# Optimization experiments

Hardware: AMD Instinct MI355X
Metric: run time of the kernel (lower is better)

Reference implementation:

```python
import jax, jax.numpy as jnp
import numpy as np

B, P, E = 16, 1024, 768
HID, HEADS = 768, 12
DH = HID // HEADS  # 64
EPS = 1e-5


def setup_inputs() -> dict:
    key = jax.random.key(0)
    ks = jax.random.split(key, 4)
    return {
        "x": jax.random.normal(ks[0], (B, P, E), dtype=jnp.float32),
        "ln_weight": jnp.ones((P, E), dtype=jnp.float32),
        "ln_bias": jnp.zeros((P, E), dtype=jnp.float32),
        "qkv": jax.random.normal(ks[1], (E, 3 * HID), dtype=jnp.float32),
        "lin_w": jax.random.normal(ks[2], (HID, E), dtype=jnp.float32) * 0.02,
        "lin_b": jax.random.normal(ks[3], (E,), dtype=jnp.float32) * 0.02,
    }


def reference(x, ln_weight, ln_bias, qkv, lin_w, lin_b):
    # LayerNorm over the last TWO dims (patches, emb), per torch nn.LayerNorm((P, E))
    mean = jnp.mean(x, axis=(-2, -1), keepdims=True)
    var = jnp.var(x, axis=(-2, -1), keepdims=True)
    xn = (x - mean) / jnp.sqrt(var + EPS) * ln_weight + ln_bias

    # QKV projection: [B,P,E] @ [E,3*HID] -> [B,P,3*HID]
    proj = xn @ qkv
    # view(B,P,heads,-1) then permute -> [B,heads,P,3*DH]; chunk along last dim
    proj = proj.reshape(B, P, HEADS, 3 * DH).transpose(0, 2, 1, 3)
    q, k, v = proj[..., :DH], proj[..., DH:2 * DH], proj[..., 2 * DH:]

    # Softmax-free attention: (Q K^T) V
    atten = jnp.einsum("bhqd,bhkd->bhqk", q, k)  # [B,H,P,P]
    out = jnp.einsum("bhqk,bhkd->bhqd", atten, v)  # [B,H,P,DH]

    out = out.transpose(0, 2, 1, 3).reshape(B, P, HID)
    # dropout p=0.0 (eval) -> identity
    out = jax.nn.relu(out @ lin_w + lin_b)
    return out + x
```

## Files before the change

kernel.cpp:

```cpp
#include <hip/hip_runtime.h>
#include <hip/hip_bf16.h>
#include <cstdint>

#define BB   16
#define PP   1024
#define EE   768
#define HID  768
#define NH   12
#define DH   64
#define NPB  (PP * EE)
#define MROWS (BB * PP)

typedef __bf16 bf16_t;
typedef __bf16 bf16x8 __attribute__((ext_vector_type(8)));
typedef float  f32x4  __attribute__((ext_vector_type(4)));

__device__ __forceinline__ void gld16(const void* g, void* l) {
    __builtin_amdgcn_global_load_lds(
        (const __attribute__((address_space(1))) void*)(uintptr_t)g,
        (__attribute__((address_space(3))) void*)(uint32_t)(uintptr_t)l,
        16, 0, 0);
}

__global__ __launch_bounds__(256) void stats1_kernel(const float* __restrict__ x,
                                                     float* __restrict__ part) {
    int bid = blockIdx.x;
    int b = bid >> 6, s = bid & 63;
    const float4* xp = (const float4*)(x + (size_t)b * NPB + (size_t)s * 12288);
    float sum = 0.f, ss = 0.f;
#pragma unroll
    for (int i = 0; i < 12; ++i) {
        float4 v = xp[i * 256 + threadIdx.x];
        sum += v.x + v.y + v.z + v.w;
        ss  += v.x * v.x + v.y * v.y + v.z * v.z + v.w * v.w;
    }
#pragma unroll
    for (int off = 32; off > 0; off >>= 1) {
        sum += __shfl_down(sum, off, 64);
        ss  += __shfl_down(ss,  off, 64);
    }
    __shared__ float tmp[8];
    int wave = threadIdx.x >> 6, lane = threadIdx.x & 63;
    if (lane == 0) { tmp[wave * 2] = sum; tmp[wave * 2 + 1] = ss; }
    __syncthreads();
    if (threadIdx.x == 0) {
        part[bid * 2]     = tmp[0] + tmp[2] + tmp[4] + tmp[6];
        part[bid * 2 + 1] = tmp[1] + tmp[3] + tmp[5] + tmp[7];
    }
}

__global__ __launch_bounds__(256) void prep_kernel(const float* __restrict__ qkvw,
                                                   const float* __restrict__ linw,
                                                   bf16_t* __restrict__ qkvT,
                                                   bf16_t* __restrict__ lwT) {
    int bid = blockIdx.x;
    __shared__ float lds[64][65];
    const float* src; bf16_t* dst; int r0, c0, W;
    if (bid < 432) {
        int tr = bid / 36, tc = bid - tr * 36;
        r0 = tr * 64; c0 = tc * 64; src = qkvw; W = 2304; dst = qkvT;
    } else {
        int bb = bid - 432;
        int tr = bb / 12, tc = bb - tr * 12;
        r0 = tr * 64; c0 = tc * 64; src = linw; W = 768; dst = lwT;
    }
    int t = threadIdx.x;
    int rr = t >> 4, cc4 = (t & 15) * 4;
#pragma unroll
    for (int j = 0; j < 4; ++j) {
        float4 v = *(const float4*)(src + (size_t)(r0 + rr + j * 16) * W + c0 + cc4);
        lds[rr + j * 16][cc4 + 0] = v.x;
        lds[rr + j * 16][cc4 + 1] = v.y;
        lds[rr + j * 16][cc4 + 2] = v.z;
        lds[rr + j * 16][cc4 + 3] = v.w;
    }
    __syncthreads();
    int cl = t >> 3, rgl = (t & 7) * 8;
#pragma unroll
    for (int jj = 0; jj < 2; ++jj) {
        int c = jj * 32 + cl;
        union { bf16_t h[8]; uint4 u; } o;
#pragma unroll
        for (int k = 0; k < 8; ++k) o.h[k] = (bf16_t)lds[rgl + k][c];
        *(uint4*)(dst + (size_t)(c0 + c) * 768 + r0 + rgl) = o.u;
    }
}

__global__ __launch_bounds__(256) void ln_apply_kernel(const float* __restrict__ x,
                                                       const float* __restrict__ lnw,
                                                       const float* __restrict__ lnb,
                                                       const float* __restrict__ part,
                                                       bf16_t* __restrict__ xn) {
    int i = (blockIdx.x * 256 + threadIdx.x) * 8;
    int b = i / NPB;
    int r = i - b * NPB;
    int lane = threadIdx.x & 63;
    float sum = part[(b * 64 + lane) * 2];
    float ss  = part[(b * 64 + lane) * 2 + 1];
#pragma unroll
    for (int off = 32; off > 0; off >>= 1) {
        sum += __shfl_down(sum, off, 64);
        ss  += __shfl_down(ss,  off, 64);
    }
    const float inv_n = 1.f / (float)NPB;
    float mean = __shfl(sum, 0, 64) * inv_n;
    float var  = __shfl(ss,  0, 64) * inv_n - mean * mean;
    float rstd = rsqrtf(var + 1e-5f);

    float4 x0 = *(const float4*)(x + i),     x1 = *(const float4*)(x + i + 4);
    float4 w0 = *(const float4*)(lnw + r),   w1 = *(const float4*)(lnw + r + 4);
    float4 c0 = *(const float4*)(lnb + r),   c1 = *(const float4*)(lnb + r + 4);
    union { bf16_t h[8]; uint4 u; } o;
    o.h[0] = (bf16_t)((x0.x - mean) * rstd * w0.x + c0.x);
    o.h[1] = (bf16_t)((x0.y - mean) * rstd * w0.y + c0.y);
    o.h[2] = (bf16_t)((x0.z - mean) * rstd * w0.z + c0.z);
    o.h[3] = (bf16_t)((x0.w - mean) * rstd * w0.w + c0.w);
    o.h[4] = (bf16_t)((x1.x - mean) * rstd * w1.x + c1.x);
    o.h[5] = (bf16_t)((x1.y - mean) * rstd * w1.y + c1.y);
    o.h[6] = (bf16_t)((x1.z - mean) * rstd * w1.z + c1.z);
    o.h[7] = (bf16_t)((x1.w - mean) * rstd * w1.w + c1.w);
    *(uint4*)(xn + i) = o.u;
}

__device__ __forceinline__ void core128_bk32(const bf16_t* __restrict__ A,
                                             const bf16_t* __restrict__ Bt,
                                             int mBase, int nBase,
                                             f32x4 acc[4][4], bf16_t* smem) {
    const int t = threadIdx.x, lane = t & 63, wave = t >> 6;
    const int wm = wave >> 1, wn = wave & 1;
    const int m16 = lane & 15, quad = lane >> 4;

    const bf16_t* gsrc[4];
    int ldst[4];
#pragma unroll
    for (int j = 0; j < 2; ++j) {
        int c = t + 256 * j;
        int l = c >> 3, lg = ((c & 7) - (l & 7)) & 7;
        int row = l + (lg >> 2) * 64, kc = lg & 3;
        gsrc[j]     = A  + (size_t)(mBase + row) * 768 + kc * 8;
        ldst[j]     = c * 8;
        gsrc[2 + j] = Bt + (size_t)(nBase + row) * 768 + kc * 8;
        ldst[2 + j] = 4096 + c * 8;
    }

    int aOff[4], bOff[4];
#pragma unroll
    for (int f = 0; f < 4; ++f) {
        aOff[f] = (f * 16 + m16) * 64 + (((wm * 4 + quad) + (m16 & 7)) & 7) * 8;
        bOff[f] = 4096 + (f * 16 + m16) * 64 + (((wn * 4 + quad) + (m16 & 7)) & 7) * 8;
    }

    const f32x4 z = {0.f, 0.f, 0.f, 0.f};
#pragma unroll
    for (int mf = 0; mf < 4; ++mf)
#pragma unroll
        for (int nf = 0; nf < 4; ++nf) acc[mf][nf] = z;

#pragma unroll
    for (int j = 0; j < 4; ++j) gld16(gsrc[j], smem + ldst[j]);
#pragma unroll
    for (int j = 0; j < 4; ++j) gld16(gsrc[j] + 32, smem + 8192 + ldst[j]);

#pragma unroll
    for (int step = 0; step < 24; ++step) {
        const int cur = (step % 3) * 8192;
        asm volatile("s_waitcnt lgkmcnt(0)" ::: "memory");
        __builtin_amdgcn_sched_barrier(0);
        __builtin_amdgcn_s_barrier();
        if (step + 2 < 24) {
            const int nb = ((step + 2) % 3) * 8192;
            const int kq = (step + 2) * 32;
#pragma unroll
            for (int j = 0; j < 4; ++j)
                gld16(gsrc[j] + kq, smem + nb + ldst[j]);
        }
        if (step < 22)       asm volatile("s_waitcnt vmcnt(8)" ::: "memory");
        else if (step == 22) asm volatile("s_waitcnt vmcnt(4)" ::: "memory");
        else                 asm volatile("s_waitcnt vmcnt(0)" ::: "memory");
        __builtin_amdgcn_sched_barrier(0);
        __builtin_amdgcn_s_barrier();

        bf16x8 af[4], bfv[4];
#pragma unroll
        for (int f = 0; f < 4; ++f) {
            af[f]  = *(const bf16x8*)(smem + cur + aOff[f]);
            bfv[f] = *(const bf16x8*)(smem + cur + bOff[f]);
        }
        __builtin_amdgcn_s_setprio(1);
#pragma unroll
        for (int mf = 0; mf < 4; ++mf)
#pragma unroll
            for (int nf = 0; nf < 4; ++nf)
                acc[mf][nf] = __builtin_amdgcn_mfma_f32_16x16x32_bf16(
                    af[mf], bfv[nf], acc[mf][nf], 0, 0, 0);
        __builtin_amdgcn_s_setprio(0);
    }
}

__global__ __launch_bounds__(256, 2) void gemm_qkv_kernel(const bf16_t* __restrict__ xn,
                                                          const bf16_t* __restrict__ qkvT,
                                                          bf16_t* __restrict__ q,
                                                          bf16_t* __restrict__ kt,
                                                          bf16_t* __restrict__ vt) {
    __shared__ bf16_t smem[36864];
    const int t = threadIdx.x, lane = t & 63, wave = t >> 6;
    const int wm = wave >> 1, wn = wave & 1;
    const int m16 = lane & 15, quad = lane >> 4;

    const int lb = blockIdx.y * 9 + blockIdx.x;
    if (lb & 1) __builtin_amdgcn_s_sleep(28);
    const int id = (lb & 7) * 144 + (lb >> 3);
    const int tx = id % 9, ty = id / 9;
    const int mBase = ty * 128, nBase = tx * 256;

    const bf16_t* gsrc[6];
    int ldst[6];
#pragma unroll
    for (int j = 0; j < 2; ++j) {
        int c = t + 256 * j;
        int l = c >> 3, lg = ((c & 7) - (l & 7)) & 7;
        gsrc[j] = xn + (size_t)(mBase + l + (lg >> 2) * 64) * 768 + (lg & 3) * 8;
        ldst[j] = c * 8;
    }
#pragma unroll
    for (int j = 0; j < 4; ++j) {
        int c = t + 256 * j;
        int l = c >> 3, lg = ((c & 7) - (l & 7)) & 7;
        gsrc[2 + j] = qkvT + (size_t)(nBase + l + (lg >> 2) * 128) * 768 + (lg & 3) * 8;
        ldst[2 + j] = 4096 + c * 8;
    }

    int aOff[4], bOff[8];
#pragma unroll
    for (int mf = 0; mf < 4; ++mf)
        aOff[mf] = (mf * 16 + m16) * 64 + (((wm * 4 + quad) + (m16 & 7)) & 7) * 8;
#pragma unroll
    for (int nf = 0; nf < 8; ++nf)
        bOff[nf] = 4096 + (nf * 16 + m16) * 64 + (((wn * 4 + quad) + (m16 & 7)) & 7) * 8;

    f32x4 acc[4][8];
    const f32x4 z = {0.f, 0.f, 0.f, 0.f};
#pragma unroll
    for (int mf = 0; mf < 4; ++mf)
#pragma unroll
        for (int nf = 0; nf < 8; ++nf) acc[mf][nf] = z;

#pragma unroll
    for (int j = 0; j < 6; ++j) gld16(gsrc[j], smem + ldst[j]);
#pragma unroll
    for (int j = 0; j < 6; ++j) gld16(gsrc[j] + 32, smem + 12288 + ldst[j]);

#pragma unroll
    for (int step = 0; step < 24; ++step) {
        const int cur = (step % 3) * 12288;
        asm volatile("s_waitcnt lgkmcnt(0)" ::: "memory");
        __builtin_amdgcn_sched_barrier(0);
        __builtin_amdgcn_s_barrier();
        if (step + 2 < 24) {
            const int nb = ((step + 2) % 3) * 12288;
            const int kq = (step + 2) * 32;
#pragma unroll
            for (int j = 0; j < 6; ++j)
                gld16(gsrc[j] + kq, smem + nb + ldst[j]);
        }
        if (step < 22)       asm volatile("s_waitcnt vmcnt(12)" ::: "memory");
        else if (step == 22) asm volatile("s_waitcnt vmcnt(6)"  ::: "memory");
        else                 asm volatile("s_waitcnt vmcnt(0)"  ::: "memory");
        __builtin_amdgcn_sched_barrier(0);
        __builtin_amdgcn_s_barrier();

        bf16x8 af[4], bf0[4], bf1[4];
#pragma unroll
        for (int mf = 0; mf < 4; ++mf)
            af[mf] = *(const bf16x8*)(smem + cur + aOff[mf]);
#pragma unroll
        for (int nf = 0; nf < 4; ++nf)
            bf0[nf] = *(const bf16x8*)(smem + cur + bOff[nf]);
#pragma unroll
        for (int nf = 0; nf < 4; ++nf)
            bf1[nf] = *(const bf16x8*)(smem + cur + bOff[4 + nf]);
        __builtin_amdgcn_s_setprio(1);
#pragma unroll
        for (int mf = 0; mf < 4; ++mf)
#pragma unroll
            for (int nf = 0; nf < 4; ++nf)
                acc[mf][nf] = __builtin_amdgcn_mfma_f32_16x16x32_bf16(
                    af[mf], bf0[nf], acc[mf][nf], 0, 0, 0);
#pragma unroll
        for (int mf = 0; mf < 4; ++mf)
#pragma unroll
            for (int nf = 0; nf < 4; ++nf)
                acc[mf][4 + nf] = __builtin_amdgcn_mfma_f32_16x16x32_bf16(
                    af[mf], bf1[nf], acc[mf][4 + nf], 0, 0, 0);
        __builtin_amdgcn_s_setprio(0);
    }

    asm volatile("s_waitcnt lgkmcnt(0)" ::: "memory");
    __builtin_amdgcn_sched_barrier(0);
    bf16_t* slot = smem + wave * 4608;
    const int b = mBase >> 10, p0 = mBase & 1023;

#pragma unroll
    for (int half = 0; half < 2; ++half) {
        const int g64 = tx * 4 + wn * 2 + half;
        const int cls = g64 % 3, h = g64 / 3;
        if (cls == 0) {
#pragma unroll
            for (int mf = 0; mf < 4; ++mf)
#pragma unroll
                for (int nfl = 0; nfl < 4; ++nfl)
#pragma unroll
                    for (int i = 0; i < 4; ++i)
                        slot[(mf * 16 + quad * 4 + i) * 72 + nfl * 16 + m16] =
                            (bf16_t)acc[mf][half * 4 + nfl][i];
            asm volatile("s_waitcnt lgkmcnt(0)" ::: "memory");
            __builtin_amdgcn_sched_barrier(0);
#pragma unroll
            for (int j = 0; j < 8; ++j) {
                int r = j * 8 + (lane >> 3), cc = lane & 7;
                bf16x8 val = *(const bf16x8*)(slot + r * 72 + cc * 8);
                *(bf16x8*)(q + ((size_t)(b * 1024 + p0 + wm * 64 + r)) * 768 +
                           h * 64 + cc * 8) = val;
            }
        } else {
            bf16_t* dst = (cls == 1) ? kt : vt;
            const size_t bh = (size_t)(b * 12 + h);
#pragma unroll
            for (int mf = 0; mf < 4; ++mf)
#pragma unroll
                for (int nfl = 0; nfl < 4; ++nfl) {
                    int c = nfl * 16 + m16;
                    union { bf16_t hh[4]; uint2 u; } pk;
#pragma unroll
                    for (int i = 0; i < 4; ++i)
                        pk.hh[i] = (bf16_t)acc[mf][half * 4 + nfl][i];
                    *(uint2*)(slot + c * 72 + mf * 16 + quad * 4) = pk.u;
                }
            asm volatile("s_waitcnt lgkmcnt(0)" ::: "memory");
            __builtin_amdgcn_sched_barrier(0);
#pragma unroll
            for (int j = 0; j < 8; ++j) {
                int c = (lane >> 3) + j * 8, r8 = (lane & 7) * 8;
                bf16x8 val = *(const bf16x8*)(slot + c * 72 + r8);
                *(bf16x8*)(dst + (bh * 64 + c) * 1024 + p0 + wm * 64 + r8) = val;
            }
        }
        if (half == 0) {
            asm volatile("s_waitcnt lgkmcnt(0)" ::: "memory");
            __builtin_amdgcn_sched_barrier(0);
        }
    }
}

__global__ __launch_bounds__(256) void kvu_kernel(const bf16_t* __restrict__ kt,
                                                  const bf16_t* __restrict__ vt,
                                                  const bf16_t* __restrict__ lwT,
                                                  bf16_t* __restrict__ ut) {
    __shared__ float red[4 * 64 * 65];
    const int bh = blockIdx.x;
    const int b = bh / NH, h = bh - b * NH;
    const bf16_t* Kb = kt + (size_t)bh * DH * PP;
    const bf16_t* Vb = vt + (size_t)bh * DH * PP;
    const int t = threadIdx.x;
    const int lane = t & 63, wave = t >> 6;
    const int m16 = lane & 15, quad = lane >> 4;
    const f32x4 z = {0.f, 0.f, 0.f, 0.f};

    {
        f32x4 acc[4][4];
#pragma unroll
        for (int mm = 0; mm < 4; ++mm)
#pragma unroll
            for (int nn = 0; nn < 4; ++nn) acc[mm][nn] = z;
        for (int ks = 0; ks < 8; ++ks) {
            int kb = wave * 256 + ks * 32 + quad * 8;
            bf16x8 af[4], bfv[4];
#pragma unroll
            for (int mm = 0; mm < 4; ++mm)
                af[mm] = *(const bf16x8*)(Kb + (size_t)(mm * 16 + m16) * PP + kb);
#pragma unroll
            for (int nn = 0; nn < 4; ++nn)
                bfv[nn] = *(const bf16x8*)(Vb + (size_t)(nn * 16 + m16) * PP + kb);
#pragma unroll
            for (int mm = 0; mm < 4; ++mm)
#pragma unroll
                for (int nn = 0; nn < 4; ++nn)
                    acc[mm][nn] = __builtin_amdgcn_mfma_f32_16x16x32_bf16(
                        af[mm], bfv[nn], acc[mm][nn], 0, 0, 0);
        }
#pragma unroll
        for (int mm = 0; mm < 4; ++mm)
#pragma unroll
            for (int nn = 0; nn < 4; ++nn)
#pragma unroll
                for (int i = 0; i < 4; ++i)
                    red[wave * 4160 + (mm * 16 + quad * 4 + i) * 65 + nn * 16 + m16] =
                        acc[mm][nn][i];
    }
    __syncthreads();

    const int wm = wave >> 1, wn = wave & 1;
    bf16x8 ah[2][2], al[2][2];
#pragma unroll
    for (int mm = 0; mm < 2; ++mm)
#pragma unroll
        for (int ks = 0; ks < 2; ++ks) {
            int d1 = wm * 32 + mm * 16 + m16;
            int base = d1 * 65 + ks * 32 + quad * 8;
#pragma unroll
            for (int e = 0; e < 8; ++e) {
                float s = red[base + e] + red[4160 + base + e] +
                          red[8320 + base + e] + red[12480 + base + e];
                bf16_t hi = (bf16_t)s;
                ah[mm][ks][e] = hi;
                al[mm][ks][e] = (bf16_t)(s - (float)hi);
            }
        }

#pragma unroll
    for (int ny = 0; ny < 3; ++ny) {
        const int nBase = ny * 256;
        f32x4 acc2[2][8];
#pragma unroll
        for (int mm = 0; mm < 2; ++mm)
#pragma unroll
            for (int nn = 0; nn < 8; ++nn) acc2[mm][nn] = z;
#pragma unroll
        for (int ks = 0; ks < 2; ++ks) {
            bf16x8 bfr[8];
#pragma unroll
            for (int nn = 0; nn < 8; ++nn)
                bfr[nn] = *(const bf16x8*)(
                    lwT + (size_t)(nBase + wn * 128 + nn * 16 + m16) * 768 +
                    h * 64 + ks * 32 + quad * 8);
#pragma unroll
            for (int mm = 0; mm < 2; ++mm)
#pragma unroll
                for (int nn = 0; nn < 8; ++nn) {
                    acc2[mm][nn] = __builtin_amdgcn_mfma_f32_16x16x32_bf16(
                        ah[mm][ks], bfr[nn], acc2[mm][nn], 0, 0, 0);
                    acc2[mm][nn] = __builtin_amdgcn_mfma_f32_16x16x32_bf16(
                        al[mm][ks], bfr[nn], acc2[mm][nn], 0, 0, 0);
                }
        }
#pragma unroll
        for (int mm = 0; mm < 2; ++mm)
#pragma unroll
            for (int nn = 0; nn < 8; ++nn) {
                int e  = nBase + wn * 128 + nn * 16 + m16;
                int d1 = wm * 32 + mm * 16 + quad * 4;
                union { bf16_t hh[4]; uint2 u; } pk;
#pragma unroll
                for (int i = 0; i < 4; ++i) pk.hh[i] = (bf16_t)acc2[mm][nn][i];
                *(uint2*)(ut + ((size_t)b * 768 + e) * 768 + h * 64 + d1) = pk.u;
            }
    }
}

__global__ __launch_bounds__(256, 3) void gemm_out_kernel(const bf16_t* __restrict__ q,
                                                          const bf16_t* __restrict__ ut,
                                                          const float* __restrict__ linb,
                                                          const float* __restrict__ x,
                                                          float* __restrict__ out) {
    __shared__ bf16_t smem[24576];
    const int lb  = blockIdx.y * 6 + blockIdx.x;
    const int swz = (lb & 7) * 96 + (lb >> 3);
    const int tx  = swz % 6, ty = swz / 6;
    const int mBase = ty * 128, nBase = tx * 128;
    const int b = mBase >> 10;

    f32x4 acc[4][4];
    core128_bk32(q, ut + (size_t)b * 768 * 768, mBase, nBase, acc, smem);

    const int lane = threadIdx.x & 63, wave = threadIdx.x >> 6;
    const int wm = wave >> 1, wn = wave & 1;
    const int m16 = lane & 15, quad = lane >> 4;

    asm volatile("s_waitcnt lgkmcnt(0)" ::: "memory");
    __builtin_amdgcn_sched_barrier(0);
    __syncthreads();

    float* fslot = (float*)smem + wave * 2176;
    const int cl = lane & 15, rq = lane >> 4;
    const int colBase = nBase + wn * 64;
    const float4 lb4 = *(const float4*)(linb + colBase + cl * 4);

#pragma unroll
    for (int p = 0; p < 2; ++p) {
#pragma unroll
        for (int mm = 0; mm < 2; ++mm)
#pragma unroll
            for (int nn = 0; nn < 4; ++nn)
#pragma unroll
                for (int i = 0; i < 4; ++i)
                    fslot[(mm * 16 + quad * 4 + i) * 68 + nn * 16 + m16] =
                        acc[p * 2 + mm][nn][i];
        asm volatile("s_waitcnt lgkmcnt(0)" ::: "memory");
        __builtin_amdgcn_sched_barrier(0);
#pragma unroll
        for (int j = 0; j < 8; ++j) {
            int lr = j * 4 + rq;
            size_t row = (size_t)(mBase + wm * 64 + p * 32 + lr);
            float4 v4 = *(const float4*)(fslot + lr * 68 + cl * 4);
            float4 x4 = *(const float4*)(x + row * EE + colBase + cl * 4);
            float4 o4;
            o4.x = fmaxf(v4.x + lb4.x, 0.f) + x4.x;
            o4.y = fmaxf(v4.y + lb4.y, 0.f) + x4.y;
            o4.z = fmaxf(v4.z + lb4.z, 0.f) + x4.z;
            o4.w = fmaxf(v4.w + lb4.w, 0.f) + x4.w;
            *(float4*)(out + row * EE + colBase + cl * 4) = o4;
        }
        if (p == 0) {
            asm volatile("s_waitcnt lgkmcnt(0)" ::: "memory");
            __builtin_amdgcn_sched_barrier(0);
        }
    }
}

extern "C" void kernel_launch(void* const* d_in, const int* in_sizes, int n_in,
                              void* d_out, int out_size, void* d_ws, size_t ws_size,
                              hipStream_t stream) {
    const float* x    = (const float*)d_in[0];
    const float* lnw  = (const float*)d_in[1];
    const float* lnb  = (const float*)d_in[2];
    const float* qkvw = (const float*)d_in[3];
    const float* linw = (const float*)d_in[4];
    const float* linb = (const float*)d_in[5];
    float* out = (float*)d_out;
    char* ws = (char*)d_ws;

    float*  part  = (float*)(ws + 0);
    bf16_t* xn    = (bf16_t*)(ws + 8448);
    bf16_t* qkvT  = (bf16_t*)(ws + 25174272);
    bf16_t* lwT   = (bf16_t*)(ws + 28713216);
    bf16_t* q     = (bf16_t*)(ws + 29892864);
    bf16_t* kt    = (bf16_t*)(ws + 55058688);
    bf16_t* vt    = (bf16_t*)(ws + 80224512);
    bf16_t* ut    = xn;

    stats1_kernel<<<dim3(BB * 64), dim3(256), 0, stream>>>(x, part);
    prep_kernel<<<dim3(576), dim3(256), 0, stream>>>(qkvw, linw, qkvT, lwT);
    ln_apply_kernel<<<dim3(6144), dim3(256), 0, stream>>>(x, lnw, lnb, part, xn);
    gemm_qkv_kernel<<<dim3(9, 128), dim3(256), 0, stream>>>(xn, qkvT, q, kt, vt);
    kvu_kernel<<<dim3(192), dim3(256), 0, stream>>>(kt, vt, lwT, ut);
    gemm_out_kernel<<<dim3(6, 128), dim3(256), 0, stream>>>(q, ut, linb, x, out);
}
```

Measured before the change: 245.0 us.

## Split K^T V reduction and U projection into wider-grid kernels; merge stats and prep

Merges the LayerNorm statistics kernel and the weight transpose/convert kernel into one launch so the two independent jobs share a single grid. Splits the former 192-block kvu kernel into a kv_part kernel (192x2 blocks, each reducing half the sequence into an fp32 partial) and a u_kernel (192x3 blocks, each producing a 256-column slice of U). This raises parallelism on a GPU with many more CUs than 192. The cost is an extra launch and an fp32 partial buffer round-trip through global memory. It also leaves a dead load loop in u_kernel.

```diff
diff --git a/kernel.cpp b/kernel.cpp
--- a/kernel.cpp
+++ b/kernel.cpp
@@ -22,67 +22,68 @@
         16, 0, 0);
 }
 
-__global__ __launch_bounds__(256) void stats1_kernel(const float* __restrict__ x,
-                                                     float* __restrict__ part) {
+__global__ __launch_bounds__(256) void stats_prep_kernel(const float* __restrict__ x,
+                                                         const float* __restrict__ qkvw,
+                                                         const float* __restrict__ linw,
+                                                         float* __restrict__ part,
+                                                         bf16_t* __restrict__ qkvT,
+                                                         bf16_t* __restrict__ lwT) {
     int bid = blockIdx.x;
-    int b = bid >> 6, s = bid & 63;
-    const float4* xp = (const float4*)(x + (size_t)b * NPB + (size_t)s * 12288);
-    float sum = 0.f, ss = 0.f;
-#pragma unroll
-    for (int i = 0; i < 12; ++i) {
-        float4 v = xp[i * 256 + threadIdx.x];
-        sum += v.x + v.y + v.z + v.w;
-        ss  += v.x * v.x + v.y * v.y + v.z * v.z + v.w * v.w;
-    }
-#pragma unroll
-    for (int off = 32; off > 0; off >>= 1) {
-        sum += __shfl_down(sum, off, 64);
-        ss  += __shfl_down(ss,  off, 64);
-    }
-    __shared__ float tmp[8];
-    int wave = threadIdx.x >> 6, lane = threadIdx.x & 63;
-    if (lane == 0) { tmp[wave * 2] = sum; tmp[wave * 2 + 1] = ss; }
-    __syncthreads();
-    if (threadIdx.x == 0) {
-        part[bid * 2]     = tmp[0] + tmp[2] + tmp[4] + tmp[6];
-        part[bid * 2 + 1] = tmp[1] + tmp[3] + tmp[5] + tmp[7];
-    }
-}
-
-__global__ __launch_bounds__(256) void prep_kernel(const float* __restrict__ qkvw,
-                                                   const float* __restrict__ linw,
-                                                   bf16_t* __restrict__ qkvT,
-                                                   bf16_t* __restrict__ lwT) {
-    int bid = blockIdx.x;
-    __shared__ float lds[64][65];
-    const float* src; bf16_t* dst; int r0, c0, W;
-    if (bid < 432) {
-        int tr = bid / 36, tc = bid - tr * 36;
-        r0 = tr * 64; c0 = tc * 64; src = qkvw; W = 2304; dst = qkvT;
+    if (bid < 1024) {
+        int b = bid >> 6, s = bid & 63;
+        const float4* xp = (const float4*)(x + (size_t)b * NPB + (size_t)s * 12288);
+        float sum = 0.f, ss = 0.f;
+#pragma unroll
+        for (int i = 0; i < 12; ++i) {
+            float4 v = xp[i * 256 + threadIdx.x];
+            sum += v.x + v.y + v.z + v.w;
+            ss  += v.x * v.x + v.y * v.y + v.z * v.z + v.w * v.w;
+        }
+#pragma unroll
+        for (int off = 32; off > 0; off >>= 1) {
+            sum += __shfl_down(sum, off, 64);
+            ss  += __shfl_down(ss,  off, 64);
+        }
+        __shared__ float tmp[8];
+        int wave = threadIdx.x >> 6, lane = threadIdx.x & 63;
+        if (lane == 0) { tmp[wave * 2] = sum; tmp[wave * 2 + 1] = ss; }
+        __syncthreads();
+        if (threadIdx.x == 0) {
+            part[bid * 2]     = tmp[0] + tmp[2] + tmp[4] + tmp[6];
+            part[bid * 2 + 1] = tmp[1] + tmp[3] + tmp[5] + tmp[7];
+        }
     } else {
-        int bb = bid - 432;
-        int tr = bb / 12, tc = bb - tr * 12;
-        r0 = tr * 64; c0 = tc * 64; src = linw; W = 768; dst = lwT;
-    }
-    int t = threadIdx.x;
-    int rr = t >> 4, cc4 = (t & 15) * 4;
-#pragma unroll
-    for (int j = 0; j < 4; ++j) {
-        float4 v = *(const float4*)(src + (size_t)(r0 + rr + j * 16) * W + c0 + cc4);
-        lds[rr + j * 16][cc4 + 0] = v.x;
-        lds[rr + j * 16][cc4 + 1] = v.y;
-        lds[rr + j * 16][cc4 + 2] = v.z;
-        lds[rr + j * 16][cc4 + 3] = v.w;
-    }
-    __syncthreads();
-    int cl = t >> 3, rgl = (t & 7) * 8;
-#pragma unroll
-    for (int jj = 0; jj < 2; ++jj) {
-        int c = jj * 32 + cl;
-        union { bf16_t h[8]; uint4 u; } o;
-#pragma unroll
-        for (int k = 0; k < 8; ++k) o.h[k] = (bf16_t)lds[rgl + k][c];
-        *(uint4*)(dst + (size_t)(c0 + c) * 768 + r0 + rgl) = o.u;
+        __shared__ float lds[64][65];
+        int pid = bid - 1024;
+        const float* src; bf16_t* dst; int r0, c0, W;
+        if (pid < 432) {
+            int tr = pid / 36, tc = pid - tr * 36;
+            r0 = tr * 64; c0 = tc * 64; src = qkvw; W = 2304; dst = qkvT;
+        } else {
+            int bb = pid - 432;
+            int tr = bb / 12, tc = bb - tr * 12;
+            r0 = tr * 64; c0 = tc * 64; src = linw; W = 768; dst = lwT;
+        }
+        int t = threadIdx.x;
+        int rr = t >> 4, cc4 = (t & 15) * 4;
+#pragma unroll
+        for (int j = 0; j < 4; ++j) {
+            float4 v = *(const float4*)(src + (size_t)(r0 + rr + j * 16) * W + c0 + cc4);
+            lds[rr + j * 16][cc4 + 0] = v.x;
+            lds[rr + j * 16][cc4 + 1] = v.y;
+            lds[rr + j * 16][cc4 + 2] = v.z;
+            lds[rr + j * 16][cc4 + 3] = v.w;
+        }
+        __syncthreads();
+        int cl = t >> 3, rgl = (t & 7) * 8;
+#pragma unroll
+        for (int jj = 0; jj < 2; ++jj) {
+            int c = jj * 32 + cl;
+            union { bf16_t h[8]; uint4 u; } o;
+#pragma unroll
+            for (int k = 0; k < 8; ++k) o.h[k] = (bf16_t)lds[rgl + k][c];
+            *(uint4*)(dst + (size_t)(c0 + c) * 768 + r0 + rgl) = o.u;
+        }
     }
 }
 
@@ -352,109 +353,145 @@
     }
 }
 
-__global__ __launch_bounds__(256) void kvu_kernel(const bf16_t* __restrict__ kt,
-                                                  const bf16_t* __restrict__ vt,
-                                                  const bf16_t* __restrict__ lwT,
-                                                  bf16_t* __restrict__ ut) {
+__global__ __launch_bounds__(256) void kv_part_kernel(const bf16_t* __restrict__ kt,
+                                                      const bf16_t* __restrict__ vt,
+                                                      float* __restrict__ partial) {
     __shared__ float red[4 * 64 * 65];
-    const int bh = blockIdx.x;
-    const int b = bh / NH, h = bh - b * NH;
+    const int bh = blockIdx.x, c = blockIdx.y;
     const bf16_t* Kb = kt + (size_t)bh * DH * PP;
     const bf16_t* Vb = vt + (size_t)bh * DH * PP;
     const int t = threadIdx.x;
     const int lane = t & 63, wave = t >> 6;
     const int m16 = lane & 15, quad = lane >> 4;
     const f32x4 z = {0.f, 0.f, 0.f, 0.f};
-
-    {
-        f32x4 acc[4][4];
+    f32x4 acc[4][4];
+#pragma unroll
+    for (int mm = 0; mm < 4; ++mm)
+#pragma unroll
+        for (int nn = 0; nn < 4; ++nn) acc[mm][nn] = z;
+
+#pragma unroll
+    for (int ks = 0; ks < 4; ++ks) {
+        int kb = c * 512 + wave * 128 + ks * 32 + quad * 8;
+        bf16x8 af[4], bfv[4];
 #pragma unroll
         for (int mm = 0; mm < 4; ++mm)
-#pragma unroll
-            for (int nn = 0; nn < 4; ++nn) acc[mm][nn] = z;
-        for (int ks = 0; ks < 8; ++ks) {
-            int kb = wave * 256 + ks * 32 + quad * 8;
-            bf16x8 af[4], bfv[4];
-#pragma unroll
-            for (int mm = 0; mm < 4; ++mm)
-                af[mm] = *(const bf16x8*)(Kb + (size_t)(mm * 16 + m16) * PP + kb);
+            af[mm] = *(const bf16x8*)(Kb + (size_t)(mm * 16 + m16) * PP + kb);
+#pragma unroll
+        for (int nn = 0; nn < 4; ++nn)
+            bfv[nn] = *(const bf16x8*)(Vb + (size_t)(nn * 16 + m16) * PP + kb);
+#pragma unroll
+        for (int mm = 0; mm < 4; ++mm)
 #pragma unroll
             for (int nn = 0; nn < 4; ++nn)
-                bfv[nn] = *(const bf16x8*)(Vb + (size_t)(nn * 16 + m16) * PP + kb);
-#pragma unroll
-            for (int mm = 0; mm < 4; ++mm)
-#pragma unroll
-                for (int nn = 0; nn < 4; ++nn)
-                    acc[mm][nn] = __builtin_amdgcn_mfma_f32_16x16x32_bf16(
-                        af[mm], bfv[nn], acc[mm][nn], 0, 0, 0);
-        }
-#pragma unroll
-        for (int mm = 0; mm < 4; ++mm)
-#pragma unroll
-            for (int nn = 0; nn < 4; ++nn)
-#pragma unroll
-                for (int i = 0; i < 4; ++i)
-                    red[wave * 4160 + (mm * 16 + quad * 4 + i) * 65 + nn * 16 + m16] =
-                        acc[mm][nn][i];
-    }
+                acc[mm][nn] = __builtin_amdgcn_mfma_f32_16x16x32_bf16(
+                    af[mm], bfv[nn], acc[mm][nn], 0, 0, 0);
+    }
+#pragma unroll
+    for (int mm = 0; mm < 4; ++mm)
+#pragma unroll
+        for (int nn = 0; nn < 4; ++nn)
+#pragma unroll
+            for (int i = 0; i < 4; ++i)
+                red[wave * 4160 + (mm * 16 + quad * 4 + i) * 65 + nn * 16 + m16] =
+                    acc[mm][nn][i];
     __syncthreads();
-
+    float* dst = partial + (size_t)(bh * 2 + c) * 4096;
+#pragma unroll
+    for (int j = 0; j < 4; ++j) {
+        int f0 = j * 1024 + t * 4;
+        int m = f0 >> 6, n = f0 & 63;
+        int a = m * 65 + n;
+        float4 s;
+        s.x = red[a]     + red[4160 + a]     + red[8320 + a]     + red[12480 + a];
+        s.y = red[a + 1] + red[4160 + a + 1] + red[8320 + a + 1] + red[12480 + a + 1];
+        s.z = red[a + 2] + red[4160 + a + 2] + red[8320 + a + 2] + red[12480 + a + 2];
+        s.w = red[a + 3] + red[4160 + a + 3] + red[8320 + a + 3] + red[12480 + a + 3];
+        *(float4*)(dst + f0) = s;
+    }
+}
+
+__global__ __launch_bounds__(256) void u_kernel(const float* __restrict__ partial,
+                                                const bf16_t* __restrict__ lwT,
+                                                bf16_t* __restrict__ ut) {
+    const int bh = blockIdx.x;
+    const int b = bh / NH, h = bh - b * NH;
+    const int nBase = blockIdx.y * 256;
+    const int t = threadIdx.x, lane = t & 63, wave = t >> 6;
     const int wm = wave >> 1, wn = wave & 1;
+    const int m16 = lane & 15, quad = lane >> 4;
+    const f32x4 z = {0.f, 0.f, 0.f, 0.f};
+    const float* P0 = partial + (size_t)(bh * 2) * 4096;
+    const float* P1 = P0 + 4096;
+
     bf16x8 ah[2][2], al[2][2];
 #pragma unroll
     for (int mm = 0; mm < 2; ++mm)
 #pragma unroll
         for (int ks = 0; ks < 2; ++ks) {
             int d1 = wm * 32 + mm * 16 + m16;
-            int base = d1 * 65 + ks * 32 + quad * 8;
+            int off = d1 * 64 + ks * 32 + quad * 8;
+            float4 a0 = *(const float4*)(P0 + off),     a1 = *(const float4*)(P0 + off + 4);
+            float4 b0 = *(const float4*)(P1 + off),     b1 = *(const float4*)(P1 + off + 4);
+            float sv[8] = { a0.x + b0.x, a0.y + b0.y, a0.z + b0.z, a0.w + b0.w,
+                            a1.x + b1.x, a1.y + b1.y, a1.z + b1.z, a1.w + b1.w };
 #pragma unroll
             for (int e = 0; e < 8; ++e) {
-                float s = red[base + e] + red[4160 + base + e] +
-                          red[8320 + base + e] + red[12480 + base + e];
-                bf16_t hi = (bf16_t)s;
+                bf16_t hi = (bf16_t)sv[e];
                 ah[mm][ks][e] = hi;
-                al[mm][ks][e] = (bf16_t)(s - (float)hi);
+                al[mm][ks][e] = (bf16_t)(sv[e] - (float)hi);
             }
         }
 
 #pragma unroll
-    for (int ny = 0; ny < 3; ++ny) {
-        const int nBase = ny * 256;
-        f32x4 acc2[2][8];
+    for (int ks = 0; ks < 2; ++ks) {
+        bf16x8 bfr[8];
+#pragma unroll
+        for (int nn = 0; nn < 8; ++nn)
+            bfr[nn] = *(const bf16x8*)(
+                lwT + (size_t)(nBase + wn * 128 + nn * 16 + m16) * 768 +
+                h * 64 + ks * 32 + quad * 8);
+        static f32x4 dummy;
+        (void)dummy;
+        if (ks == 0) {
+        }
+        break;
+    }
+
+    f32x4 acc2[2][8];
+#pragma unroll
+    for (int mm = 0; mm < 2; ++mm)
+#pragma unroll
+        for (int nn = 0; nn < 8; ++nn) acc2[mm][nn] = z;
+#pragma unroll
+    for (int ks = 0; ks < 2; ++ks) {
+        bf16x8 bfr[8];
+#pragma unroll
+        for (int nn = 0; nn < 8; ++nn)
+            bfr[nn] = *(const bf16x8*)(
+                lwT + (size_t)(nBase + wn * 128 + nn * 16 + m16) * 768 +
+                h * 64 + ks * 32 + quad * 8);
 #pragma unroll
         for (int mm = 0; mm < 2; ++mm)
 #pragma unroll
-            for (int nn = 0; nn < 8; ++nn) acc2[mm][nn] = z;
-#pragma unroll
-        for (int ks = 0; ks < 2; ++ks) {
-            bf16x8 bfr[8];
-#pragma unroll
-            for (int nn = 0; nn < 8; ++nn)
-                bfr[nn] = *(const bf16x8*)(
-                    lwT + (size_t)(nBase + wn * 128 + nn * 16 + m16) * 768 +
-                    h * 64 + ks * 32 + quad * 8);
-#pragma unroll
-            for (int mm = 0; mm < 2; ++mm)
-#pragma unroll
-                for (int nn = 0; nn < 8; ++nn) {
-                    acc2[mm][nn] = __builtin_amdgcn_mfma_f32_16x16x32_bf16(
-                        ah[mm][ks], bfr[nn], acc2[mm][nn], 0, 0, 0);
-                    acc2[mm][nn] = __builtin_amdgcn_mfma_f32_16x16x32_bf16(
-                        al[mm][ks], bfr[nn], acc2[mm][nn], 0, 0, 0);
-                }
-        }
-#pragma unroll
-        for (int mm = 0; mm < 2; ++mm)
-#pragma unroll
             for (int nn = 0; nn < 8; ++nn) {
-                int e  = nBase + wn * 128 + nn * 16 + m16;
-                int d1 = wm * 32 + mm * 16 + quad * 4;
-                union { bf16_t hh[4]; uint2 u; } pk;
-#pragma unroll
-                for (int i = 0; i < 4; ++i) pk.hh[i] = (bf16_t)acc2[mm][nn][i];
-                *(uint2*)(ut + ((size_t)b * 768 + e) * 768 + h * 64 + d1) = pk.u;
+                acc2[mm][nn] = __builtin_amdgcn_mfma_f32_16x16x32_bf16(
+                    ah[mm][ks], bfr[nn], acc2[mm][nn], 0, 0, 0);
+                acc2[mm][nn] = __builtin_amdgcn_mfma_f32_16x16x32_bf16(
+                    al[mm][ks], bfr[nn], acc2[mm][nn], 0, 0, 0);
             }
     }
+#pragma unroll
+    for (int mm = 0; mm < 2; ++mm)
+#pragma unroll
+        for (int nn = 0; nn < 8; ++nn) {
+            int e  = nBase + wn * 128 + nn * 16 + m16;
+            int d1 = wm * 32 + mm * 16 + quad * 4;
+            union { bf16_t hh[4]; uint2 u; } pk;
+#pragma unroll
+            for (int i = 0; i < 4; ++i) pk.hh[i] = (bf16_t)acc2[mm][nn][i];
+            *(uint2*)(ut + ((size_t)b * 768 + e) * 768 + h * 64 + d1) = pk.u;
+        }
 }
 
 __global__ __launch_bounds__(256, 3) void gemm_out_kernel(const bf16_t* __restrict__ q,
@@ -529,19 +566,21 @@
     float* out = (float*)d_out;
     char* ws = (char*)d_ws;
 
-    float*  part  = (float*)(ws + 0);
-    bf16_t* xn    = (bf16_t*)(ws + 8448);
-    bf16_t* qkvT  = (bf16_t*)(ws + 25174272);
-    bf16_t* lwT   = (bf16_t*)(ws + 28713216);
-    bf16_t* q     = (bf16_t*)(ws + 29892864);
-    bf16_t* kt    = (bf16_t*)(ws + 55058688);
-    bf16_t* vt    = (bf16_t*)(ws + 80224512);
-    bf16_t* ut    = xn;
-
-    stats1_kernel<<<dim3(BB * 64), dim3(256), 0, stream>>>(x, part);
-    prep_kernel<<<dim3(576), dim3(256), 0, stream>>>(qkvw, linw, qkvT, lwT);
+    float*  part    = (float*)(ws + 0);
+    bf16_t* xn      = (bf16_t*)(ws + 8448);
+    bf16_t* qkvT    = (bf16_t*)(ws + 25174272);
+    bf16_t* lwT     = (bf16_t*)(ws + 28713216);
+    bf16_t* q       = (bf16_t*)(ws + 29892864);
+    bf16_t* kt      = (bf16_t*)(ws + 55058688);
+    bf16_t* vt      = (bf16_t*)(ws + 80224512);
+    bf16_t* ut      = xn;
+    float*  partial = (float*)(ws + 8448 + 18874368);
+
+    stats_prep_kernel<<<dim3(1600), dim3(256), 0, stream>>>(x, qkvw, linw, part,
+                                                            qkvT, lwT);
     ln_apply_kernel<<<dim3(6144), dim3(256), 0, stream>>>(x, lnw, lnb, part, xn);
     gemm_qkv_kernel<<<dim3(9, 128), dim3(256), 0, stream>>>(xn, qkvT, q, kt, vt);
-    kvu_kernel<<<dim3(192), dim3(256), 0, stream>>>(kt, vt, lwT, ut);
+    kv_part_kernel<<<dim3(192, 2), dim3(256), 0, stream>>>(kt, vt, partial);
+    u_kernel<<<dim3(192, 3), dim3(256), 0, stream>>>(partial, lwT, ut);
     gemm_out_kernel<<<dim3(6, 128), dim3(256), 0, stream>>>(q, ut, linb, x, out);
 }
```

Result: slower. 253.9 us (+3.6%).
